# Kernel tuning notes

Hardware: AMD Instinct MI355X
Metric: run time of the kernel (lower is better)

Reference implementation:

```python
import jax, jax.numpy as jnp
import numpy as np

D = 128          # input_dim
H = 512          # hidden_dim = max(64, 4*D)
C = 10           # n_classes
T = 15           # n_trees
DEPTH = 3        # tree_depth
I = 2 ** DEPTH - 1   # n_internal = 7
L = 2 ** DEPTH       # n_leaves = 8
PPT = I * (D + 1) + L * C   # params_per_tree = 983
P = T * PPT                  # total_params = 14745
LN_EPS = 1e-5
B_TRAIN = 100000
B_TEST = 100000


def setup_inputs() -> dict:
    key = jax.random.key(0)
    ks = jax.random.split(key, 16)
    s = 0.02
    return {
        "X_train": jax.random.normal(ks[0], (B_TRAIN, D), jnp.float32),
        "X_test": jax.random.normal(ks[1], (B_TEST, D), jnp.float32),
        "enc_W1": jax.random.normal(ks[2], (H, D), jnp.float32) * s,
        "enc_b1": jnp.zeros((H,), jnp.float32),
        "ln1_g": jnp.ones((H,), jnp.float32),
        "ln1_b": jnp.zeros((H,), jnp.float32),
        "enc_W2": jax.random.normal(ks[3], (H, H), jnp.float32) * s,
        "enc_b2": jnp.zeros((H,), jnp.float32),
        "ln2_g": jnp.ones((H,), jnp.float32),
        "ln2_b": jnp.zeros((H,), jnp.float32),
        "head_W1": jax.random.normal(ks[4], (C, H, H), jnp.float32) * s,
        "head_b1": jnp.zeros((C, H), jnp.float32),
        "head_W2": jax.random.normal(ks[5], (C, P, H), jnp.float32) * s,
        "head_b2": jax.random.normal(ks[6], (C, P), jnp.float32) * s,
        "tree_weights": jnp.ones((T,), jnp.float32) / T,
    }


def _layernorm(x, g, b):
    m = x.mean(-1, keepdims=True)
    v = ((x - m) ** 2).mean(-1, keepdims=True)
    return (x - m) * jax.lax.rsqrt(v + LN_EPS) * g + b


def reference(X_train, X_test, enc_W1, enc_b1, ln1_g, ln1_b, enc_W2, enc_b2,
              ln2_g, ln2_b, head_W1, head_b1, head_W2, head_b2, tree_weights):
    # data encoder on the train-mean vector (dropout is identity in eval)
    mean = X_train.mean(0)                                  # [D]
    h = jax.nn.relu(_layernorm(enc_W1 @ mean + enc_b1, ln1_g, ln1_b))
    h = jax.nn.relu(_layernorm(enc_W2 @ h + enc_b2, ln2_g, ln2_b))   # [H]

    # all class heads at once: params [C, P]
    hh = jax.nn.relu(jnp.einsum('chd,d->ch', head_W1, h) + head_b1)
    params = jnp.einsum('cph,ch->cp', head_W2, hh) + head_b2

    # unpack per-tree params: [C, T, ...]
    p = params.reshape(C, T, PPT)
    split_w = p[..., :I * D].reshape(C, T, I, D)
    split_b = p[..., I * D:I * D + I]                       # [C, T, I]
    leaf_logits = p[..., I * D + I:].reshape(C, T, L, C)

    # soft routing (only the first DEPTH internal nodes are used, as in the source)
    routes = jax.nn.sigmoid(
        jnp.einsum('bd,ctid->ctbi', X_test, split_w) + split_b[:, :, None, :]
    )                                                       # [C, T, B, I]
    lp = jnp.ones(routes.shape[:3] + (1,), routes.dtype)    # [C, T, B, 1]
    for d in range(DEPTH):
        left = routes[..., d:d + 1]
        lp = jnp.concatenate([lp * left, lp * (1.0 - left)], axis=-1)
    # lp: [C, T, B, L]

    tree_out = jax.nn.softmax(leaf_logits, axis=-1)         # [C, T, L, C]
    probs = jnp.einsum('ctbl,ctlk->ctbk', lp[..., :L], tree_out)
    w = jax.nn.softmax(tree_weights)                        # [T]
    ens = jnp.einsum('t,ctbk->cbk', w, probs)               # per-head ensemble
    return ens.mean(0)                                      # [B, C]
```

## Files before the change

kernel.cpp:

```cpp
#include <hip/hip_runtime.h>

#define DD 128
#define NC 10
#define NT 15
#define NCT 150
#define NCOLS 450
#define BTRAIN 100000
#define BTEST 100000
#define GROWS 70050
#define NGRP 38

typedef __attribute__((ext_vector_type(8))) __bf16 bf16x8;
typedef __attribute__((ext_vector_type(4))) float f32x4;
typedef __attribute__((ext_vector_type(8))) unsigned short u16x8;

static __device__ __forceinline__ unsigned short f2bf(float f) {
  unsigned int u = __builtin_bit_cast(unsigned int, f);
  u = (u + 0x7FFFu + ((u >> 16) & 1u)) >> 16;
  return (unsigned short)u;
}

__global__ void __launch_bounds__(256) k_colsum(const float* __restrict__ X, float* __restrict__ partial) {
  int tid = threadIdx.x;
  int gid = blockIdx.x * 256 + tid;
  int stride = gridDim.x * 256;
  float sx = 0.f, sy = 0.f, sz = 0.f, sw = 0.f;
  const float4* Xv = (const float4*)X;
  for (int i = gid; i < BTRAIN * 32; i += stride) {
    float4 v = Xv[i];
    sx += v.x; sy += v.y; sz += v.z; sw += v.w;
  }
  __shared__ float red[256][4];
  red[tid][0] = sx; red[tid][1] = sy; red[tid][2] = sz; red[tid][3] = sw;
  __syncthreads();
  for (int off = 128; off >= 32; off >>= 1) {
    if (tid < off) {
      red[tid][0] += red[tid + off][0];
      red[tid][1] += red[tid + off][1];
      red[tid][2] += red[tid + off][2];
      red[tid][3] += red[tid + off][3];
    }
    __syncthreads();
  }
  if (tid < 32) {
#pragma unroll
    for (int i = 0; i < 4; ++i)
      partial[blockIdx.x * 128 + tid * 4 + i] = red[tid][i];
  }
}

__global__ void __launch_bounds__(512) k_enc1(const float* __restrict__ partial, const float* __restrict__ W1,
                                              const float* __restrict__ b1, const float* __restrict__ g,
                                              const float* __restrict__ bb, float* __restrict__ out) {
  __shared__ float mS[DD];
  __shared__ float red[512];
  int t = threadIdx.x;
  {
    int c = t & 127, qd = t >> 7;
    float s = 0.0f;
    const float* pp = partial + (size_t)qd * 128 * 128 + c;
    for (int k = 0; k < 128; ++k) s += pp[k * 128];
    red[t] = s; __syncthreads();
    if (t < 128) mS[t] = (red[t] + red[t + 128] + red[t + 256] + red[t + 384]) * (1.0f / BTRAIN);
    __syncthreads();
  }
  float z = b1[t];
  const float4* w = (const float4*)(W1 + t * DD);
#pragma unroll
  for (int j = 0; j < DD / 4; ++j) {
    float4 wv = w[j];
    z += wv.x * mS[4 * j] + wv.y * mS[4 * j + 1] + wv.z * mS[4 * j + 2] + wv.w * mS[4 * j + 3];
  }
  __syncthreads();
  red[t] = z; __syncthreads();
  for (int off = 256; off > 0; off >>= 1) { if (t < off) red[t] += red[t + off]; __syncthreads(); }
  float m = red[0] * (1.0f / 512.0f); __syncthreads();
  float d = z - m;
  red[t] = d * d; __syncthreads();
  for (int off = 256; off > 0; off >>= 1) { if (t < off) red[t] += red[t + off]; __syncthreads(); }
  float v = red[0] * (1.0f / 512.0f);
  out[t] = fmaxf(d * rsqrtf(v + 1e-5f) * g[t] + bb[t], 0.0f);
}

template <int RELU>
__global__ void __launch_bounds__(256) k_matvec512(const float* __restrict__ W, const float* __restrict__ x,
                                                   const float* __restrict__ bias, float* __restrict__ out, int rows) {
  int wv = threadIdx.x >> 6, lane = threadIdx.x & 63;
  int row = blockIdx.x * 4 + wv;
  if (row >= rows) return;
  const float4* wr = (const float4*)(W + (size_t)row * 512) + lane * 2;
  const float4* xv = (const float4*)x + lane * 2;
  float4 a0 = wr[0], a1 = wr[1], x0 = xv[0], x1 = xv[1];
  float s = a0.x * x0.x + a0.y * x0.y + a0.z * x0.z + a0.w * x0.w
          + a1.x * x1.x + a1.y * x1.y + a1.z * x1.z + a1.w * x1.w;
#pragma unroll
  for (int off = 32; off > 0; off >>= 1) s += __shfl_down(s, off);
  if (lane == 0) {
    s += bias[row];
    if (RELU) s = fmaxf(s, 0.0f);
    out[row] = s;
  }
}

__global__ void __launch_bounds__(512) k_ln(const float* __restrict__ z, const float* __restrict__ g,
                                            const float* __restrict__ bb, float* __restrict__ out) {
  __shared__ float red[512];
  int t = threadIdx.x;
  float zv = z[t];
  red[t] = zv; __syncthreads();
  for (int off = 256; off > 0; off >>= 1) { if (t < off) red[t] += red[t + off]; __syncthreads(); }
  float m = red[0] * (1.0f / 512.0f); __syncthreads();
  float d = zv - m;
  red[t] = d * d; __syncthreads();
  for (int off = 256; off > 0; off >>= 1) { if (t < off) red[t] += red[t + off]; __syncthreads(); }
  float v = red[0] * (1.0f / 512.0f);
  out[t] = fmaxf(d * rsqrtf(v + 1e-5f) * g[t] + bb[t], 0.0f);
}

__global__ void __launch_bounds__(256) k_params(const float* __restrict__ W2, const float* __restrict__ hh,
                                                const float* __restrict__ b2, unsigned short* __restrict__ Wb,
                                                float* __restrict__ sb, float* __restrict__ leaf) {
  int wv = threadIdx.x >> 6, lane = threadIdx.x & 63;
  int base = (blockIdx.x * 4 + wv) * 8;
  if (base >= GROWS) return;
  float4 a[8][2];
  size_t rowoff[8];
  int ctArr[8], wArr[8], cArr[8];
#pragma unroll
  for (int i = 0; i < 8; ++i) {
    int R = base + i;
    if (R >= GROWS) R = GROWS - 1;
    int ctIdx = R / 467;
    int w = R - ctIdx * 467;
    int c = ctIdx / 15;
    int t = ctIdx - c * 15;
    int p;
    if (w < 384) p = t * 983 + w;
    else if (w < 387) p = t * 983 + 896 + (w - 384);
    else p = t * 983 + 903 + (w - 387);
    rowoff[i] = (size_t)c * 14745 + p;
    ctArr[i] = ctIdx; wArr[i] = w; cArr[i] = c;
    const float4* wr = (const float4*)(W2 + rowoff[i] * 512) + lane * 2;
    a[i][0] = wr[0];
    a[i][1] = wr[1];
  }
#pragma unroll
  for (int i = 0; i < 8; ++i) {
    const float4* xv = (const float4*)(hh + cArr[i] * 512) + lane * 2;
    float4 x0 = xv[0], x1 = xv[1];
    float s = a[i][0].x * x0.x + a[i][0].y * x0.y + a[i][0].z * x0.z + a[i][0].w * x0.w
            + a[i][1].x * x1.x + a[i][1].y * x1.y + a[i][1].z * x1.z + a[i][1].w * x1.w;
#pragma unroll
    for (int off = 32; off > 0; off >>= 1) s += __shfl_down(s, off);
    if (lane == 0) {
      s += b2[rowoff[i]];
      int w = wArr[i], ctIdx = ctArr[i];
      if (w < 384) {
        int ii = w >> 7, d = w & 127;
        Wb[(size_t)(ctIdx * 3 + ii) * DD + d] = f2bf(s);
      } else if (w < 387) {
        sb[ctIdx * 3 + (w - 384)] = s;
      } else {
        leaf[ctIdx * 80 + (w - 387)] = s;
      }
    }
  }
}

__global__ void k_tob(const float* __restrict__ leaf, const float* __restrict__ tw, unsigned short* __restrict__ TOB) {
  int g = blockIdx.x;
  int lane = threadIdx.x;
  int ct = g * 4 + (lane >> 4);
  int cls = lane & 15;
  float mx = tw[0];
  for (int i = 1; i < 15; ++i) mx = fmaxf(mx, tw[i]);
  float wsum = 0.0f;
  for (int i = 0; i < 15; ++i) wsum += __expf(tw[i] - mx);
  u16x8 o;
#pragma unroll
  for (int j = 0; j < 8; ++j) {
    float v = 0.0f;
    if (ct < NCT && cls < NC) {
      float wt = __expf(tw[ct % 15] - mx) / wsum;
      const float* lr = leaf + ct * 80 + j * 10;
      float m2 = lr[0];
#pragma unroll
      for (int k = 1; k < 10; ++k) m2 = fmaxf(m2, lr[k]);
      float es = 0.0f;
#pragma unroll
      for (int k = 0; k < 10; ++k) es += __expf(lr[k] - m2);
      v = __expf(lr[cls] - m2) / es * wt * (1.0f / (float)NC);
    }
    o[j] = f2bf(v);
  }
  *(u16x8*)&TOB[((size_t)g * 64 + lane) * 8] = o;
}

__global__ void __launch_bounds__(256) k_fused(const float* __restrict__ X, const unsigned short* __restrict__ Wb,
                                               const float* __restrict__ sb, const unsigned short* __restrict__ TOB,
                                               float* __restrict__ out) {
  __shared__ union {
    unsigned short Xs[64][152];
    _Float16 Rs[64][242];
  } sU;
  int tid = threadIdx.x;
  int b0 = blockIdx.x * 64;
  {
    int row = tid >> 2, seg = tid & 3;
    int gb = b0 + row;
    const float4* xr = (const float4*)(X + (size_t)gb * DD) + seg * 8;
#pragma unroll
    for (int j2 = 0; j2 < 4; ++j2) {
      u16x8 u;
      if (gb < BTEST) {
        float4 va = xr[2 * j2], vb = xr[2 * j2 + 1];
        u[0] = f2bf(va.x); u[1] = f2bf(va.y); u[2] = f2bf(va.z); u[3] = f2bf(va.w);
        u[4] = f2bf(vb.x); u[5] = f2bf(vb.y); u[6] = f2bf(vb.z); u[7] = f2bf(vb.w);
      } else {
#pragma unroll
        for (int j = 0; j < 8; ++j) u[j] = 0;
      }
      *(u16x8*)&sU.Xs[row][seg * 32 + j2 * 8] = u;
    }
  }
  __syncthreads();
  int wv = tid >> 6, lane = tid & 63;
  int m = lane & 15, g = lane >> 4;
  bf16x8 A[4][4];
#pragma unroll
  for (int rt = 0; rt < 4; ++rt)
#pragma unroll
    for (int ks = 0; ks < 4; ++ks)
      A[rt][ks] = __builtin_bit_cast(bf16x8, *(const u16x8*)&sU.Xs[rt * 16 + m][ks * 32 + g * 8]);
  __syncthreads();
  f32x4 accA = 0.0f, accB = 0.0f;
  int pl = wv * 16 + m;
#pragma unroll
  for (int pass = 0; pass < 2; ++pass) {
    int passBase = pass ? 240 : 0;
    {
      int tstart, tcnt;
      if (pass == 0) { tstart = wv * 4; tcnt = (wv == 3) ? 3 : 4; }
      else { tstart = 15 + ((wv < 2) ? wv * 4 : (8 + (wv - 2) * 3)); tcnt = (wv < 2) ? 4 : 3; }
      int col = tstart * 16 + m;
      u16x8 Bv[4];
#pragma unroll
      for (int ks = 0; ks < 4; ++ks)
        Bv[ks] = *(const u16x8*)&Wb[(size_t)col * DD + ks * 32 + g * 8];
      float sbv = sb[col];
      for (int it = 0; it < tcnt; ++it) {
        int pc = (it + 1 < tcnt) ? (col + 16) : col;
        u16x8 Bn[4];
#pragma unroll
        for (int ks = 0; ks < 4; ++ks)
          Bn[ks] = *(const u16x8*)&Wb[(size_t)pc * DD + ks * 32 + g * 8];
        float sbn = sb[pc];
        f32x4 acc[4];
#pragma unroll
        for (int rt = 0; rt < 4; ++rt) acc[rt] = 0.0f;
#pragma unroll
        for (int ks = 0; ks < 4; ++ks) {
          bf16x8 Bf = __builtin_bit_cast(bf16x8, Bv[ks]);
#pragma unroll
          for (int rt = 0; rt < 4; ++rt)
            acc[rt] = __builtin_amdgcn_mfma_f32_16x16x32_bf16(A[rt][ks], Bf, acc[rt], 0, 0, 0);
        }
        int colLocal = col - passBase;
#pragma unroll
        for (int rt = 0; rt < 4; ++rt)
#pragma unroll
          for (int r = 0; r < 4; ++r) {
            float pre = acc[rt][r] + sbv;
            float sg = 1.0f / (1.0f + __expf(-pre));
            sU.Rs[rt * 16 + g * 4 + r][colLocal] = (_Float16)sg;
          }
#pragma unroll
        for (int ks = 0; ks < 4; ++ks) Bv[ks] = Bn[ks];
        sbv = sbn;
        col += 16;
      }
    }
    __syncthreads();
    {
      int gbase = pass ? 20 : 0;
      int gn = pass ? 18 : 20;
      int ctl = g;
      for (int gi = 0; gi < gn; ++gi) {
        int gAbs = gbase + gi;
        int ct = gAbs * 4 + ctl;
        int cb = 3 * ct - passBase;
        float l0 = (float)sU.Rs[pl][cb + 0];
        float l1 = (float)sU.Rs[pl][cb + 1];
        float l2 = (float)sU.Rs[pl][cb + 2];
        float n0 = 1.0f - l0, n1 = 1.0f - l1, n2 = 1.0f - l2;
        float p00 = l1 * l0, p01 = l1 * n0, p10 = n1 * l0, p11 = n1 * n0;
        float lp[8] = { l2 * p00, l2 * p01, l2 * p10, l2 * p11,
                        n2 * p00, n2 * p01, n2 * p10, n2 * p11 };
        bool valid = (ct < NCT);
        u16x8 av;
#pragma unroll
        for (int j = 0; j < 8; ++j) av[j] = valid ? f2bf(lp[j]) : (unsigned short)0;
        u16x8 bv = *(const u16x8*)&TOB[((size_t)gAbs * 64 + lane) * 8];
        if (gi & 1)
          accB = __builtin_amdgcn_mfma_f32_16x16x32_bf16(__builtin_bit_cast(bf16x8, av),
                                                         __builtin_bit_cast(bf16x8, bv), accB, 0, 0, 0);
        else
          accA = __builtin_amdgcn_mfma_f32_16x16x32_bf16(__builtin_bit_cast(bf16x8, av),
                                                         __builtin_bit_cast(bf16x8, bv), accA, 0, 0, 0);
      }
    }
    __syncthreads();
  }
  f32x4 accT = accA + accB;
  int cls = lane & 15;
  if (cls < NC) {
#pragma unroll
    for (int r = 0; r < 4; ++r) {
      int b = b0 + wv * 16 + (lane >> 4) * 4 + r;
      if (b < BTEST) out[(size_t)b * 10 + cls] = accT[r];
    }
  }
}

extern "C" void kernel_launch(void* const* d_in, const int* in_sizes, int n_in,
                              void* d_out, int out_size, void* d_ws, size_t ws_size,
                              hipStream_t stream) {
  const float* Xtr = (const float*)d_in[0];
  const float* Xte = (const float*)d_in[1];
  const float* eW1 = (const float*)d_in[2];
  const float* eb1 = (const float*)d_in[3];
  const float* g1  = (const float*)d_in[4];
  const float* bb1 = (const float*)d_in[5];
  const float* eW2 = (const float*)d_in[6];
  const float* eb2 = (const float*)d_in[7];
  const float* g2  = (const float*)d_in[8];
  const float* bb2 = (const float*)d_in[9];
  const float* hW1 = (const float*)d_in[10];
  const float* hb1 = (const float*)d_in[11];
  const float* hW2 = (const float*)d_in[12];
  const float* hb2 = (const float*)d_in[13];
  const float* tw  = (const float*)d_in[14];

  char* ws = (char*)d_ws;
  const size_t OFF_PART = 0;
  const size_t OFF_H1   = 262144;
  const size_t OFF_Z2   = 264192;
  const size_t OFF_H2   = 266240;
  const size_t OFF_HH   = 268288;
  const size_t OFF_LEAF = 288768;
  const size_t OFF_SB   = 336896;
  const size_t OFF_WB   = 338944;
  const size_t OFF_TOB  = 457728;
  const size_t NEED     = 496640;
  if (ws_size < NEED) return;

  float* partial = (float*)(ws + OFF_PART);
  float* h1 = (float*)(ws + OFF_H1);
  float* z2 = (float*)(ws + OFF_Z2);
  float* h2 = (float*)(ws + OFF_H2);
  float* hhp = (float*)(ws + OFF_HH);
  float* leafp = (float*)(ws + OFF_LEAF);
  float* sbp = (float*)(ws + OFF_SB);
  unsigned short* Wb = (unsigned short*)(ws + OFF_WB);
  unsigned short* TOBp = (unsigned short*)(ws + OFF_TOB);

  k_colsum<<<512, 256, 0, stream>>>(Xtr, partial);
  k_enc1<<<1, 512, 0, stream>>>(partial, eW1, eb1, g1, bb1, h1);
  k_matvec512<0><<<128, 256, 0, stream>>>(eW2, h1, eb2, z2, 512);
  k_ln<<<1, 512, 0, stream>>>(z2, g2, bb2, h2);
  k_matvec512<1><<<1280, 256, 0, stream>>>(hW1, h2, hb1, hhp, 5120);
  k_params<<<2190, 256, 0, stream>>>(hW2, hhp, hb2, Wb, sbp, leafp);
  k_tob<<<NGRP, 64, 0, stream>>>(leafp, tw, TOBp);
  k_fused<<<1563, 256, 0, stream>>>(Xte, Wb, sbp, TOBp, (float*)d_out);
}
```

Before: 141.7 us.

## Fuse encoder layers into one kernel and software-pipeline loads in fused routing kernel

Merges the first encoder layer, the second matvec and its layernorm into a single one-block kernel, removing two launches and their global round trips. The 512x512 matvec now runs in one block where each thread reads a 2KB row, so it gets much less parallelism than the 128-block version. In k_fused, the tile loop is fully unrolled with bias values preloaded. The LDS route reads and TOB loads are prefetched one iteration ahead, and a native bf16 conversion replaces the manual rounding helper.

```diff
diff --git a/kernel.cpp b/kernel.cpp
--- a/kernel.cpp
+++ b/kernel.cpp
@@ -49,11 +49,15 @@
   }
 }
 
-__global__ void __launch_bounds__(512) k_enc1(const float* __restrict__ partial, const float* __restrict__ W1,
-                                              const float* __restrict__ b1, const float* __restrict__ g,
-                                              const float* __restrict__ bb, float* __restrict__ out) {
+__global__ void __launch_bounds__(512) k_enc(const float* __restrict__ partial,
+                                             const float* __restrict__ W1, const float* __restrict__ b1,
+                                             const float* __restrict__ g1, const float* __restrict__ bb1,
+                                             const float* __restrict__ W2, const float* __restrict__ b2,
+                                             const float* __restrict__ g2, const float* __restrict__ bb2,
+                                             float* __restrict__ out) {
   __shared__ float mS[DD];
   __shared__ float red[512];
+  __shared__ float h1S[512];
   int t = threadIdx.x;
   {
     int c = t & 127, qd = t >> 7;
@@ -65,21 +69,42 @@
     __syncthreads();
   }
   float z = b1[t];
-  const float4* w = (const float4*)(W1 + t * DD);
-#pragma unroll
-  for (int j = 0; j < DD / 4; ++j) {
-    float4 wv = w[j];
-    z += wv.x * mS[4 * j] + wv.y * mS[4 * j + 1] + wv.z * mS[4 * j + 2] + wv.w * mS[4 * j + 3];
+  {
+    const float4* w = (const float4*)(W1 + t * DD);
+#pragma unroll
+    for (int j = 0; j < DD / 4; ++j) {
+      float4 wv = w[j];
+      z += wv.x * mS[4 * j] + wv.y * mS[4 * j + 1] + wv.z * mS[4 * j + 2] + wv.w * mS[4 * j + 3];
+    }
   }
   __syncthreads();
   red[t] = z; __syncthreads();
   for (int off = 256; off > 0; off >>= 1) { if (t < off) red[t] += red[t + off]; __syncthreads(); }
-  float m = red[0] * (1.0f / 512.0f); __syncthreads();
-  float d = z - m;
-  red[t] = d * d; __syncthreads();
+  float m1 = red[0] * (1.0f / 512.0f); __syncthreads();
+  float d1 = z - m1;
+  red[t] = d1 * d1; __syncthreads();
   for (int off = 256; off > 0; off >>= 1) { if (t < off) red[t] += red[t + off]; __syncthreads(); }
-  float v = red[0] * (1.0f / 512.0f);
-  out[t] = fmaxf(d * rsqrtf(v + 1e-5f) * g[t] + bb[t], 0.0f);
+  float v1 = red[0] * (1.0f / 512.0f); __syncthreads();
+  h1S[t] = fmaxf(d1 * rsqrtf(v1 + 1e-5f) * g1[t] + bb1[t], 0.0f);
+  __syncthreads();
+  float z2 = b2[t];
+  {
+    const float4* w = (const float4*)(W2 + (size_t)t * 512);
+#pragma unroll 16
+    for (int j = 0; j < 128; ++j) {
+      float4 wv = w[j];
+      z2 += wv.x * h1S[4 * j] + wv.y * h1S[4 * j + 1] + wv.z * h1S[4 * j + 2] + wv.w * h1S[4 * j + 3];
+    }
+  }
+  __syncthreads();
+  red[t] = z2; __syncthreads();
+  for (int off = 256; off > 0; off >>= 1) { if (t < off) red[t] += red[t + off]; __syncthreads(); }
+  float m2 = red[0] * (1.0f / 512.0f); __syncthreads();
+  float d2 = z2 - m2;
+  red[t] = d2 * d2; __syncthreads();
+  for (int off = 256; off > 0; off >>= 1) { if (t < off) red[t] += red[t + off]; __syncthreads(); }
+  float v2 = red[0] * (1.0f / 512.0f);
+  out[t] = fmaxf(d2 * rsqrtf(v2 + 1e-5f) * g2[t] + bb2[t], 0.0f);
 }
 
 template <int RELU>
@@ -100,21 +125,6 @@
     if (RELU) s = fmaxf(s, 0.0f);
     out[row] = s;
   }
-}
-
-__global__ void __launch_bounds__(512) k_ln(const float* __restrict__ z, const float* __restrict__ g,
-                                            const float* __restrict__ bb, float* __restrict__ out) {
-  __shared__ float red[512];
-  int t = threadIdx.x;
-  float zv = z[t];
-  red[t] = zv; __syncthreads();
-  for (int off = 256; off > 0; off >>= 1) { if (t < off) red[t] += red[t + off]; __syncthreads(); }
-  float m = red[0] * (1.0f / 512.0f); __syncthreads();
-  float d = zv - m;
-  red[t] = d * d; __syncthreads();
-  for (int off = 256; off > 0; off >>= 1) { if (t < off) red[t] += red[t + off]; __syncthreads(); }
-  float v = red[0] * (1.0f / 512.0f);
-  out[t] = fmaxf(d * rsqrtf(v + 1e-5f) * g[t] + bb[t], 0.0f);
 }
 
 __global__ void __launch_bounds__(256) k_params(const float* __restrict__ W2, const float* __restrict__ hh,
@@ -242,42 +252,49 @@
       int tstart, tcnt;
       if (pass == 0) { tstart = wv * 4; tcnt = (wv == 3) ? 3 : 4; }
       else { tstart = 15 + ((wv < 2) ? wv * 4 : (8 + (wv - 2) * 3)); tcnt = (wv < 2) ? 4 : 3; }
-      int col = tstart * 16 + m;
+      int col0 = tstart * 16 + m;
+      float sbs[4];
+#pragma unroll
+      for (int it = 0; it < 4; ++it) {
+        int tt = (it < tcnt) ? it : (tcnt - 1);
+        sbs[it] = sb[col0 + tt * 16];
+      }
       u16x8 Bv[4];
 #pragma unroll
       for (int ks = 0; ks < 4; ++ks)
-        Bv[ks] = *(const u16x8*)&Wb[(size_t)col * DD + ks * 32 + g * 8];
-      float sbv = sb[col];
-      for (int it = 0; it < tcnt; ++it) {
-        int pc = (it + 1 < tcnt) ? (col + 16) : col;
-        u16x8 Bn[4];
-#pragma unroll
-        for (int ks = 0; ks < 4; ++ks)
-          Bn[ks] = *(const u16x8*)&Wb[(size_t)pc * DD + ks * 32 + g * 8];
-        float sbn = sb[pc];
-        f32x4 acc[4];
-#pragma unroll
-        for (int rt = 0; rt < 4; ++rt) acc[rt] = 0.0f;
-#pragma unroll
-        for (int ks = 0; ks < 4; ++ks) {
-          bf16x8 Bf = __builtin_bit_cast(bf16x8, Bv[ks]);
+        Bv[ks] = *(const u16x8*)&Wb[(size_t)col0 * DD + ks * 32 + g * 8];
+#pragma unroll
+      for (int it = 0; it < 4; ++it) {
+        if (it < tcnt) {
+          int col = col0 + it * 16;
+          int pc = (it + 1 < tcnt) ? (col + 16) : col;
+          u16x8 Bn[4];
+#pragma unroll
+          for (int ks = 0; ks < 4; ++ks)
+            Bn[ks] = *(const u16x8*)&Wb[(size_t)pc * DD + ks * 32 + g * 8];
+          f32x4 acc[4];
+#pragma unroll
+          for (int rt = 0; rt < 4; ++rt) acc[rt] = 0.0f;
+#pragma unroll
+          for (int ks = 0; ks < 4; ++ks) {
+            bf16x8 Bf = __builtin_bit_cast(bf16x8, Bv[ks]);
+#pragma unroll
+            for (int rt = 0; rt < 4; ++rt)
+              acc[rt] = __builtin_amdgcn_mfma_f32_16x16x32_bf16(A[rt][ks], Bf, acc[rt], 0, 0, 0);
+          }
+          float sbv = sbs[it];
+          int colLocal = col - passBase;
 #pragma unroll
           for (int rt = 0; rt < 4; ++rt)
-            acc[rt] = __builtin_amdgcn_mfma_f32_16x16x32_bf16(A[rt][ks], Bf, acc[rt], 0, 0, 0);
+#pragma unroll
+            for (int r = 0; r < 4; ++r) {
+              float pre = acc[rt][r] + sbv;
+              float sg = 1.0f / (1.0f + __expf(-pre));
+              sU.Rs[rt * 16 + g * 4 + r][colLocal] = (_Float16)sg;
+            }
+#pragma unroll
+          for (int ks = 0; ks < 4; ++ks) Bv[ks] = Bn[ks];
         }
-        int colLocal = col - passBase;
-#pragma unroll
-        for (int rt = 0; rt < 4; ++rt)
-#pragma unroll
-          for (int r = 0; r < 4; ++r) {
-            float pre = acc[rt][r] + sbv;
-            float sg = 1.0f / (1.0f + __expf(-pre));
-            sU.Rs[rt * 16 + g * 4 + r][colLocal] = (_Float16)sg;
-          }
-#pragma unroll
-        for (int ks = 0; ks < 4; ++ks) Bv[ks] = Bn[ks];
-        sbv = sbn;
-        col += 16;
       }
     }
     __syncthreads();
@@ -285,28 +302,39 @@
       int gbase = pass ? 20 : 0;
       int gn = pass ? 18 : 20;
       int ctl = g;
+      int ct0 = gbase * 4 + ctl;
+      int cb0 = 3 * ct0 - passBase;
+      _Float16 r0 = sU.Rs[pl][cb0 + 0];
+      _Float16 r1 = sU.Rs[pl][cb0 + 1];
+      _Float16 r2 = sU.Rs[pl][cb0 + 2];
+      u16x8 bv = *(const u16x8*)&TOB[((size_t)gbase * 64 + lane) * 8];
       for (int gi = 0; gi < gn; ++gi) {
         int gAbs = gbase + gi;
+        _Float16 s0 = r0, s1 = r1, s2 = r2;
+        u16x8 bn = bv;
+        if (gi + 1 < gn) {
+          int ctn = (gAbs + 1) * 4 + ctl;
+          int cbn = 3 * ctn - passBase;
+          s0 = sU.Rs[pl][cbn + 0];
+          s1 = sU.Rs[pl][cbn + 1];
+          s2 = sU.Rs[pl][cbn + 2];
+          bn = *(const u16x8*)&TOB[((size_t)(gAbs + 1) * 64 + lane) * 8];
+        }
         int ct = gAbs * 4 + ctl;
-        int cb = 3 * ct - passBase;
-        float l0 = (float)sU.Rs[pl][cb + 0];
-        float l1 = (float)sU.Rs[pl][cb + 1];
-        float l2 = (float)sU.Rs[pl][cb + 2];
+        float l0 = (float)r0, l1 = (float)r1, l2 = (float)r2;
         float n0 = 1.0f - l0, n1 = 1.0f - l1, n2 = 1.0f - l2;
         float p00 = l1 * l0, p01 = l1 * n0, p10 = n1 * l0, p11 = n1 * n0;
         float lp[8] = { l2 * p00, l2 * p01, l2 * p10, l2 * p11,
                         n2 * p00, n2 * p01, n2 * p10, n2 * p11 };
         bool valid = (ct < NCT);
-        u16x8 av;
-#pragma unroll
-        for (int j = 0; j < 8; ++j) av[j] = valid ? f2bf(lp[j]) : (unsigned short)0;
-        u16x8 bv = *(const u16x8*)&TOB[((size_t)gAbs * 64 + lane) * 8];
+        bf16x8 av;
+#pragma unroll
+        for (int j = 0; j < 8; ++j) av[j] = valid ? (__bf16)lp[j] : (__bf16)0.0f;
         if (gi & 1)
-          accB = __builtin_amdgcn_mfma_f32_16x16x32_bf16(__builtin_bit_cast(bf16x8, av),
-                                                         __builtin_bit_cast(bf16x8, bv), accB, 0, 0, 0);
+          accB = __builtin_amdgcn_mfma_f32_16x16x32_bf16(av, __builtin_bit_cast(bf16x8, bv), accB, 0, 0, 0);
         else
-          accA = __builtin_amdgcn_mfma_f32_16x16x32_bf16(__builtin_bit_cast(bf16x8, av),
-                                                         __builtin_bit_cast(bf16x8, bv), accA, 0, 0, 0);
+          accA = __builtin_amdgcn_mfma_f32_16x16x32_bf16(av, __builtin_bit_cast(bf16x8, bv), accA, 0, 0, 0);
+        r0 = s0; r1 = s1; r2 = s2; bv = bn;
       }
     }
     __syncthreads();
@@ -343,10 +371,8 @@
 
   char* ws = (char*)d_ws;
   const size_t OFF_PART = 0;
-  const size_t OFF_H1   = 262144;
-  const size_t OFF_Z2   = 264192;
-  const size_t OFF_H2   = 266240;
-  const size_t OFF_HH   = 268288;
+  const size_t OFF_H2   = 262144;
+  const size_t OFF_HH   = 266240;
   const size_t OFF_LEAF = 288768;
   const size_t OFF_SB   = 336896;
   const size_t OFF_WB   = 338944;
@@ -355,8 +381,6 @@
   if (ws_size < NEED) return;
 
   float* partial = (float*)(ws + OFF_PART);
-  float* h1 = (float*)(ws + OFF_H1);
-  float* z2 = (float*)(ws + OFF_Z2);
   float* h2 = (float*)(ws + OFF_H2);
   float* hhp = (float*)(ws + OFF_HH);
   float* leafp = (float*)(ws + OFF_LEAF);
@@ -365,9 +389,7 @@
   unsigned short* TOBp = (unsigned short*)(ws + OFF_TOB);
 
   k_colsum<<<512, 256, 0, stream>>>(Xtr, partial);
-  k_enc1<<<1, 512, 0, stream>>>(partial, eW1, eb1, g1, bb1, h1);
-  k_matvec512<0><<<128, 256, 0, stream>>>(eW2, h1, eb2, z2, 512);
-  k_ln<<<1, 512, 0, stream>>>(z2, g2, bb2, h2);
+  k_enc<<<1, 512, 0, stream>>>(partial, eW1, eb1, g1, bb1, eW2, eb2, g2, bb2, h2);
   k_matvec512<1><<<1280, 256, 0, stream>>>(hW1, h2, hb1, hhp, 5120);
   k_params<<<2190, 256, 0, stream>>>(hW2, hhp, hb2, Wb, sbp, leafp);
   k_tob<<<NGRP, 64, 0, stream>>>(leafp, tw, TOBp);
```

New measurement: 183.1 us. 29.3% more time.
